# Kernel tuning notes

Measured on AMD Instinct MI355X. Metric: run time of the kernel, lower is better.

## Reference

```python
import jax, jax.numpy as jnp
import numpy as np

NHEAD = 8
HEAD_DIM = 32
AREA_WIDTH = 4
H = 32   # coarse grid height (hw0_c == hw1_c, agg_scale already applied)
W = 40   # coarse grid width
C_MAX = max(H, W) * AREA_WIDTH  # max_candidate_num = 160


def _skew(t):
    # t: [N,3] -> [N,3,3] cross-product matrix
    z = jnp.zeros_like(t[:, 0])
    return jnp.stack([
        jnp.stack([z, -t[:, 2], t[:, 1]], -1),
        jnp.stack([t[:, 2], z, -t[:, 0]], -1),
        jnp.stack([-t[:, 1], t[:, 0], z], -1),
    ], -2)


def _candidate_info(K0, K1, R, t):
    # Pixel coords in (x, y) order, as kornia.create_meshgrid(..., normalized=False)
    ys, xs = jnp.meshgrid(jnp.arange(H, dtype=jnp.float32),
                          jnp.arange(W, dtype=jnp.float32), indexing='ij')
    coord = jnp.stack([xs, ys], -1).reshape(-1, 2)  # [S,2]
    S = coord.shape[0]
    # Fundamental matrix F = K1^{-T} [t]_x R K0^{-1}
    F = jnp.swapaxes(jnp.linalg.inv(K1), -1, -2) @ _skew(t) @ R @ jnp.linalg.inv(K0)
    p = jnp.concatenate([coord, jnp.ones((S, 1), jnp.float32)], -1)  # [S,3] homogeneous
    lines = jnp.einsum('nij,lj->nli', F, p)  # [N,L,3] epipolar lines a*u+b*v+c=0 in image1
    a, b, c = lines[..., 0], lines[..., 1], lines[..., 2]
    mode = jnp.abs(b) > jnp.abs(a)  # True: parametrize v = f(u); False: u = f(v)
    b_safe = jnp.where(mode, b, 1.0)
    a_safe = jnp.where(mode, 1.0, a)
    # v(u) band check
    coord_y = (-a / b_safe)[..., None] * coord[:, 0] + (-c / b_safe)[..., None]  # [N,L,S]
    within_y = (coord[:, 1] < coord_y + AREA_WIDTH / 2.0) & (coord[:, 1] > coord_y - AREA_WIDTH / 2.0)
    # u(v) band check
    coord_x = (-b / a_safe)[..., None] * coord[:, 1] + (-c / a_safe)[..., None]  # [N,L,S]
    within_x = (coord[:, 0] < coord_x + AREA_WIDTH / 2.0) & (coord[:, 0] > coord_x - AREA_WIDTH / 2.0)
    within = jnp.where(mode[..., None], within_y, within_x)  # [N,L,S]
    # gather_index: keep the C_MAX largest source indices whose mask bit is set
    idx = jnp.arange(S)
    true_idx = jnp.where(within, idx, 0)           # [N,L,S]
    true_idx = jnp.sort(true_idx, axis=-1)
    c_index = true_idx[..., -C_MAX:]               # [N,L,C]
    valid = c_index != 0                           # index 0 treated as invalid (as in original)
    return c_index, valid


def setup_inputs() -> dict:
    key = jax.random.key(0)
    kq, kk, kv = jax.random.split(key, 3)
    N = 1
    feat = NHEAD * HEAD_DIM
    query = jax.random.normal(kq, (N, H, W, feat), jnp.float32)
    key_t = jax.random.normal(kk, (N, H, W, feat), jnp.float32)
    value = jax.random.normal(kv, (N, H, W, feat), jnp.float32)
    f = 35.0
    Kmat = jnp.array([[[f, 0.0, W / 2.0], [0.0, f, H / 2.0], [0.0, 0.0, 1.0]]], jnp.float32)
    R = jnp.eye(3, dtype=jnp.float32)[None]
    t = jnp.array([[1.0, 0.15, 0.02]], jnp.float32)
    return {"query": query, "key": key_t, "value": value, "K0": Kmat, "K1": Kmat, "R": R, "t": t}


def reference(query, key, value, K0, K1, R, t):
    c_index, valid = _candidate_info(K0, K1, R, t)  # [N,L,C] int / bool (no-grad constants)
    N = query.shape[0]
    L = H * W
    q = query.reshape(N, L, NHEAD, HEAD_DIM)
    k = key.reshape(N, L, NHEAD, HEAD_DIM)
    v = value.reshape(N, L, NHEAD, HEAD_DIM)
    n_idx = jnp.arange(N)[:, None, None]
    k_g = k[n_idx, c_index]  # [N,L,C,nhead,d]
    v_g = v[n_idx, c_index]  # [N,L,C,nhead,d]
    qk = jnp.einsum('nlhd,nlchd->nlch', q, k_g)
    scale = 1.0 / jnp.sqrt(jnp.float32(HEAD_DIM))
    scores = jnp.where(valid[..., None], qk * scale, -jnp.inf)
    A = jnp.nan_to_num(jax.nn.softmax(scores, axis=2), nan=0.0)  # fully-masked rows -> 0
    return jnp.einsum('nlch,nlchd->nlhd', A, v_g)  # [N,L,nhead,d]
```

## Files before the change

### kernel.cpp

```cpp
#include <hip/hip_runtime.h>
#include <math.h>

#define NHEAD 8
#define HEAD_DIM 32
#define IMG_H 32
#define IMG_W 40
#define NPIX (IMG_H*IMG_W)
#define CMAX 160
#define NITER (CMAX/8)
#define FEAT (NHEAD*HEAD_DIM)


__device__ void np_inv3x3_f32(const float* M, float inv[3][3]) {
#pragma clang fp contract(off)
    float A[3][3]; int piv[3];
    for (int i=0;i<3;i++) { A[i][0]=M[i*3+0]; A[i][1]=M[i*3+1]; A[i][2]=M[i*3+2]; }
    for (int kk=0;kk<3;kk++) {
        int p = kk;
        float colmax = fabsf(A[kk][kk]);
        for (int i=kk+1;i<3;i++) { float vv=fabsf(A[i][kk]); if (vv>colmax){colmax=vv;p=i;} }
        piv[kk] = p;
        if (p!=kk) { for(int j=0;j<3;j++){float tmp=A[kk][j];A[kk][j]=A[p][j];A[p][j]=tmp;} }
        const float rp = 1.0f / A[kk][kk];
        for (int i=kk+1;i<3;i++) A[i][kk] = A[i][kk] * rp;
        for (int i=kk+1;i<3;i++)
            for (int j=kk+1;j<3;j++)
                A[i][j] = A[i][j] - A[i][kk]*A[kk][j];
    }
    for (int col=0; col<3; col++) {
        float b[3] = {0.f,0.f,0.f}; b[col] = 1.0f;
        for (int kk=0;kk<3;kk++) if (piv[kk]!=kk) { float tmp=b[kk]; b[kk]=b[piv[kk]]; b[piv[kk]]=tmp; }
        for (int i=1;i<3;i++)
            for (int kk=0;kk<i;kk++)
                b[i] = b[i] - A[i][kk]*b[kk];
        for (int kk=2;kk>=0;kk--) {
            b[kk] = b[kk] / A[kk][kk];
            for (int i=0;i<kk;i++)
                b[i] = b[i] - A[i][kk]*b[kk];
        }
        inv[0][col]=b[0]; inv[1][col]=b[1]; inv[2][col]=b[2];
    }
}

__device__ void mm3_chain(const float A[3][3], const float B[3][3], float C[3][3]) {
#pragma clang fp contract(off)
    for (int i=0;i<3;i++)
        for (int j=0;j<3;j++) {
            float acc = A[i][0]*B[0][j];
            acc = acc + A[i][1]*B[1][j];
            acc = acc + A[i][2]*B[2][j];
            C[i][j] = acc;
        }
}
__device__ void mm3_fma(const float A[3][3], const float B[3][3], float C[3][3]) {
#pragma clang fp contract(off)
    for (int i=0;i<3;i++)
        for (int j=0;j<3;j++) {
            float acc = A[i][0]*B[0][j];
            acc = __builtin_fmaf(A[i][1], B[1][j], acc);
            acc = __builtin_fmaf(A[i][2], B[2][j], acc);
            C[i][j] = acc;
        }
}
__device__ float einsum_row(const float Fi[3], float x, float y) {
#pragma clang fp contract(off)
    float acc = Fi[0]*x;
    acc = acc + Fi[1]*y;
    acc = acc + Fi[2]*1.0f;
    return acc;
}


__global__ __launch_bounds__(64) void geo_kernel(
    const float* __restrict__ K0, const float* __restrict__ K1,
    const float* __restrict__ R, const float* __restrict__ t,
    float4* __restrict__ geo)
{
#pragma clang fp contract(off)
    const int l = blockIdx.x * 64 + threadIdx.x;
    float i0[3][3], i1[3][3], A[3][3], B[3][3], T1[3][3], T2[3][3], F[3][3], Rm[3][3];
    np_inv3x3_f32(K0, i0);
    np_inv3x3_f32(K1, i1);
    for (int i=0;i<3;i++)
        for (int j=0;j<3;j++) { A[i][j] = i1[j][i]; Rm[i][j] = R[i*3+j]; }
    const float t0=t[0], t1=t[1], t2=t[2];
    B[0][0]=0.f;  B[0][1]=-t2;  B[0][2]=t1;
    B[1][0]=t2;   B[1][1]=0.f;  B[1][2]=-t0;
    B[2][0]=-t1;  B[2][1]=t0;   B[2][2]=0.f;
    mm3_chain(A,B,T1);
    mm3_chain(T1,Rm,T2);
    mm3_fma(T2,i0,F);

    const float xl = (float)(l % IMG_W);
    const float yl = (float)(l / IMG_W);
    const float la = einsum_row(F[0], xl, yl);
    const float lb = einsum_row(F[1], xl, yl);
    const float lc = einsum_row(F[2], xl, yl);
    const bool  mode  = fabsf(lb) > fabsf(la);
    const float denom = mode ? lb : la;
    const float slope = (mode ? -la : -lb) / denom;
    const float icpt  = (-lc) / denom;
    geo[l] = make_float4(slope, icpt, mode ? 1.0f : 0.0f, 0.0f);
}

__global__ __launch_bounds__(512) void one2many_attn(
    const float* __restrict__ q, const float* __restrict__ k, const float* __restrict__ v,
    const float4* __restrict__ geo, float* __restrict__ out)
{
#pragma clang fp contract(off)
    __shared__ float s_q[FEAT];
    __shared__ int   s_cand[CMAX];
    __shared__ int   s_cnt;

    const int l   = blockIdx.x;
    const int tid = threadIdx.x;

    if (tid < FEAT) s_q[tid] = q[l*FEAT + tid];
    if (tid == 0) s_cnt = 0;

    const float4 g = geo[l];
    const float slope = g.x;
    const float icpt  = g.y;
    const bool  mode  = (g.z != 0.0f);
    __syncthreads();

    for (int m = tid; m < NPIX; m += 512) {
        const float xm = (float)(m % IMG_W), ym = (float)(m / IMG_W);
        const float tin  = mode ? xm : ym;
        const float tchk = mode ? ym : xm;
        const float mu = slope * tin;
        const float cc = mu + icpt;
        const float hi = cc + 2.0f;
        const float lo = cc - 2.0f;
        if ((tchk < hi) && (tchk > lo) && m != 0) {
            int pos = atomicAdd(&s_cnt, 1);
            if (pos < CMAX) s_cand[pos] = m;
        }
    }
    __syncthreads();
    const int nc = min(s_cnt, CMAX);

    const int h    = tid >> 6;
    const int lane = tid & 63;
    const int grp  = lane >> 3;
    const int dj   = (lane & 7) << 2;

    const float4 q4 = *(const float4*)(s_q + h*HEAD_DIM + dj);
    const float* kh = k + h*HEAD_DIM + dj;
    const float* vh = v + h*HEAD_DIM + dj;

    int   rows[NITER];
    float sc[NITER];
    #pragma unroll
    for (int i = 0; i < NITER; i++) {
        const int ci = (i << 3) + grp;
        rows[i] = s_cand[(ci < nc) ? ci : 0];
        const float4 kk = *(const float4*)(kh + (size_t)rows[i]*FEAT);
        float p = q4.x*kk.x;
        p = __builtin_fmaf(q4.y, kk.y, p);
        p = __builtin_fmaf(q4.z, kk.z, p);
        p = __builtin_fmaf(q4.w, kk.w, p);
        p += __shfl_xor(p, 1);
        p += __shfl_xor(p, 2);
        p += __shfl_xor(p, 4);
        sc[i] = (ci < nc) ? p * 0.17677669529663687f : -INFINITY;
    }

    float mx = -INFINITY;
    #pragma unroll
    for (int i = 0; i < NITER; i++) mx = fmaxf(mx, sc[i]);
    #pragma unroll
    for (int o = 32; o; o >>= 1) mx = fmaxf(mx, __shfl_xor(mx, o));
    float losum = 0.f;
    #pragma unroll
    for (int i = 0; i < NITER; i++) {
        const float e = __expf(sc[i] - mx);
        sc[i] = e;
        losum += e;
    }
    #pragma unroll
    for (int o = 32; o; o >>= 1) losum += __shfl_xor(losum, o);
    const float sum = losum * 0.125f;

    float ax = 0.f, ay = 0.f, az = 0.f, aw = 0.f;
    #pragma unroll
    for (int i = 0; i < NITER; i++) {
        const float4 vv = *(const float4*)(vh + (size_t)rows[i]*FEAT);
        ax = __builtin_fmaf(sc[i], vv.x, ax);
        ay = __builtin_fmaf(sc[i], vv.y, ay);
        az = __builtin_fmaf(sc[i], vv.z, az);
        aw = __builtin_fmaf(sc[i], vv.w, aw);
    }
    #pragma unroll
    for (int o = 8; o <= 32; o <<= 1) {
        ax += __shfl_xor(ax, o);
        ay += __shfl_xor(ay, o);
        az += __shfl_xor(az, o);
        aw += __shfl_xor(aw, o);
    }

    if (lane < 8) {
        float4 r;
        if (nc > 0) { r.x = ax/sum; r.y = ay/sum; r.z = az/sum; r.w = aw/sum; }
        else        { r.x = r.y = r.z = r.w = 0.0f; }
        *(float4*)(out + l*FEAT + h*HEAD_DIM + dj) = r;
    }
}

extern "C" void kernel_launch(void* const* d_in, const int* in_sizes, int n_in,
                              void* d_out, int out_size, void* d_ws, size_t ws_size,
                              hipStream_t stream) {
    const float* q  = (const float*)d_in[0];
    const float* k  = (const float*)d_in[1];
    const float* v  = (const float*)d_in[2];
    const float* K0 = (const float*)d_in[3];
    const float* K1 = (const float*)d_in[4];
    const float* R  = (const float*)d_in[5];
    const float* t  = (const float*)d_in[6];
    float* out = (float*)d_out;
    float4* geo = (float4*)d_ws;
    geo_kernel<<<NPIX/64, 64, 0, stream>>>(K0, K1, R, t, geo);
    one2many_attn<<<NPIX, 512, 0, stream>>>(q, k, v, geo, out);
}
```

Measured before the change: 95.74 us.

## Enumerate epipolar band candidates analytically instead of scanning all pixels

Result: slower. 103.6 us (+8.2%).

```diff
diff --git a/kernel.cpp b/kernel.cpp
--- a/kernel.cpp
+++ b/kernel.cpp
@@ -6,8 +6,7 @@
 #define IMG_H 32
 #define IMG_W 40
 #define NPIX (IMG_H*IMG_W)
-#define CMAX 160
-#define NITER (CMAX/8)
+#define NITER 25
 #define FEAT (NHEAD*HEAD_DIM)
 
 
@@ -70,7 +69,6 @@
     return acc;
 }
 
-
 __global__ __launch_bounds__(64) void geo_kernel(
     const float* __restrict__ K0, const float* __restrict__ K1,
     const float* __restrict__ R, const float* __restrict__ t,
@@ -103,49 +101,27 @@
     geo[l] = make_float4(slope, icpt, mode ? 1.0f : 0.0f, 0.0f);
 }
 
+
 __global__ __launch_bounds__(512) void one2many_attn(
     const float* __restrict__ q, const float* __restrict__ k, const float* __restrict__ v,
     const float4* __restrict__ geo, float* __restrict__ out)
 {
 #pragma clang fp contract(off)
-    __shared__ float s_q[FEAT];
-    __shared__ int   s_cand[CMAX];
-    __shared__ int   s_cnt;
-
-    const int l   = blockIdx.x;
-    const int tid = threadIdx.x;
-
-    if (tid < FEAT) s_q[tid] = q[l*FEAT + tid];
-    if (tid == 0) s_cnt = 0;
+    const int l    = blockIdx.x;
+    const int tid  = threadIdx.x;
+    const int h    = tid >> 6;
+    const int lane = tid & 63;
+    const int grp  = lane >> 3;
+    const int dj   = (lane & 7) << 2;
 
     const float4 g = geo[l];
     const float slope = g.x;
     const float icpt  = g.y;
     const bool  mode  = (g.z != 0.0f);
-    __syncthreads();
-
-    for (int m = tid; m < NPIX; m += 512) {
-        const float xm = (float)(m % IMG_W), ym = (float)(m / IMG_W);
-        const float tin  = mode ? xm : ym;
-        const float tchk = mode ? ym : xm;
-        const float mu = slope * tin;
-        const float cc = mu + icpt;
-        const float hi = cc + 2.0f;
-        const float lo = cc - 2.0f;
-        if ((tchk < hi) && (tchk > lo) && m != 0) {
-            int pos = atomicAdd(&s_cnt, 1);
-            if (pos < CMAX) s_cand[pos] = m;
-        }
-    }
-    __syncthreads();
-    const int nc = min(s_cnt, CMAX);
-
-    const int h    = tid >> 6;
-    const int lane = tid & 63;
-    const int grp  = lane >> 3;
-    const int dj   = (lane & 7) << 2;
-
-    const float4 q4 = *(const float4*)(s_q + h*HEAD_DIM + dj);
+    const int tin_n  = mode ? IMG_W : IMG_H;
+    const int chk_n  = mode ? IMG_H : IMG_W;
+
+    const float4 q4 = *(const float4*)(q + l*FEAT + h*HEAD_DIM + dj);
     const float* kh = k + h*HEAD_DIM + dj;
     const float* vh = v + h*HEAD_DIM + dj;
 
@@ -154,8 +130,25 @@
     #pragma unroll
     for (int i = 0; i < NITER; i++) {
         const int ci = (i << 3) + grp;
-        rows[i] = s_cand[(ci < nc) ? ci : 0];
-        const float4 kk = *(const float4*)(kh + (size_t)rows[i]*FEAT);
+        const int xq = ci / 5;
+        const int pj = ci - xq*5;
+        const float tin = (float)xq;
+        const float mu  = slope * tin;
+        const float cc  = mu + icpt;
+        const float hi  = cc + 2.0f;
+        const float lo  = cc - 2.0f;
+        int yq = (int)floorf(lo) + 1 + pj;
+        yq = min(max(yq, -1), chk_n);
+        const float tchk = (float)yq;
+        const int xm = mode ? xq : yq;
+        const int ym = mode ? yq : xq;
+        int m  = ym*IMG_W + xm;
+        const bool valid = (xq < tin_n) && (yq >= 0) && (yq < chk_n)
+                        && (tchk < hi) && (tchk > lo) && (m != 0);
+        m = valid ? m : 0;
+        m = min(max(m, 0), NPIX-1);
+        rows[i] = m;
+        const float4 kk = *(const float4*)(kh + (size_t)m*FEAT);
         float p = q4.x*kk.x;
         p = __builtin_fmaf(q4.y, kk.y, p);
         p = __builtin_fmaf(q4.z, kk.z, p);
@@ -163,7 +156,7 @@
         p += __shfl_xor(p, 1);
         p += __shfl_xor(p, 2);
         p += __shfl_xor(p, 4);
-        sc[i] = (ci < nc) ? p * 0.17677669529663687f : -INFINITY;
+        sc[i] = valid ? p * 0.17677669529663687f : -INFINITY;
     }
 
     float mx = -INFINITY;
@@ -174,7 +167,7 @@
     float losum = 0.f;
     #pragma unroll
     for (int i = 0; i < NITER; i++) {
-        const float e = __expf(sc[i] - mx);
+        const float e = (sc[i] == -INFINITY) ? 0.0f : __expf(sc[i] - mx);
         sc[i] = e;
         losum += e;
     }
@@ -201,8 +194,8 @@
 
     if (lane < 8) {
         float4 r;
-        if (nc > 0) { r.x = ax/sum; r.y = ay/sum; r.z = az/sum; r.w = aw/sum; }
-        else        { r.x = r.y = r.z = r.w = 0.0f; }
+        if (mx != -INFINITY) { r.x = ax/sum; r.y = ay/sum; r.z = az/sum; r.w = aw/sum; }
+        else                 { r.x = r.y = r.z = r.w = 0.0f; }
         *(float4*)(out + l*FEAT + h*HEAD_DIM + dj) = r;
     }
 }
```
